# Performance work log

Hardware: AMD Instinct MI355X
Metric: run time of the kernel (lower is better)

The kernel has to match this reference:

```python
import jax, jax.numpy as jnp
import numpy as np

N_NODES = 100000
N_EDGES = 1200000
D_FEAT = 64
THETA = (1.0, -0.8, 0.4, -0.1)  # polynomial coefficients, k = len(THETA)


def setup_inputs() -> dict:
    key = jax.random.key(0)
    k1, k2, k3 = jax.random.split(key, 3)
    feat = jax.random.normal(k1, (N_NODES, D_FEAT), dtype=jnp.float32)
    src = jax.random.randint(k2, (N_EDGES,), 0, N_NODES, dtype=jnp.int32)
    dst = jax.random.randint(k3, (N_EDGES,), 0, N_NODES, dtype=jnp.int32)
    return {"feat": feat, "src": src, "dst": dst}


def reference(feat, src, dst):
    # in-degrees: number of incoming edges per node (clamped to >= 1)
    deg = jax.ops.segment_sum(jnp.ones((N_EDGES,), feat.dtype), dst, num_segments=N_NODES)
    d_invsqrt = jnp.clip(deg, 1.0, None) ** -0.5  # [N]
    d = d_invsqrt[:, None]  # [N, 1]

    h = THETA[0] * feat
    for k in range(1, len(THETA)):
        # unnLaplacian: feat - D^{-1/2} A^T (D^{-1/2} feat)  (copy_u / sum over edges)
        msg = (feat * d)[src]                                   # [E, F] gather
        agg = jax.ops.segment_sum(msg, dst, num_segments=N_NODES)  # [N, F] scatter-add
        feat = feat - agg * d
        h = h + THETA[k] * feat
    return h
```

## Files before the change

### kernel.cpp

```cpp
#include <hip/hip_runtime.h>

#define D_FEAT 64
#define BSHIFT 8
#define BNODES 256
#define CAP 3520
#define MAXB 512
#define CHUNK 4096

typedef float nfloat4 __attribute__((ext_vector_type(4)));

__device__ inline unsigned short f2bf(float f) {
    unsigned u = __float_as_uint(f);
    unsigned r = u + 0x7fffu + ((u >> 16) & 1u);
    return (unsigned short)(r >> 16);
}
__device__ inline float bflo(unsigned w) { return __uint_as_float(w << 16); }
__device__ inline float bfhi(unsigned w) { return __uint_as_float(w & 0xffff0000u); }

__device__ inline void unpack8(uint4 u, float* v) {
    v[0] = bflo(u.x); v[1] = bfhi(u.x);
    v[2] = bflo(u.y); v[3] = bfhi(u.y);
    v[4] = bflo(u.z); v[5] = bfhi(u.z);
    v[6] = bflo(u.w); v[7] = bfhi(u.w);
}
__device__ inline uint4 pack8(const float* v) {
    uint4 u;
    u.x = (unsigned)f2bf(v[0]) | ((unsigned)f2bf(v[1]) << 16);
    u.y = (unsigned)f2bf(v[2]) | ((unsigned)f2bf(v[3]) << 16);
    u.z = (unsigned)f2bf(v[4]) | ((unsigned)f2bf(v[5]) << 16);
    u.w = (unsigned)f2bf(v[6]) | ((unsigned)f2bf(v[7]) << 16);
    return u;
}

__global__ void initcur_kernel(int* __restrict__ cursor, int P) {
    int i = blockIdx.x * 256 + threadIdx.x;
    if (i < P) cursor[i] = i * CAP;
}

__global__ void scatter_kernel(const int* __restrict__ src, const int* __restrict__ dst,
                               int* __restrict__ cursor, unsigned* __restrict__ part,
                               int nE, int P) {
    __shared__ int lh[MAXB];
    __shared__ int lcur[MAXB];
    int tid = threadIdx.x;
    for (int i = tid; i < P; i += 256) lh[i] = 0;
    __syncthreads();
    int s = blockIdx.x * CHUNK;
    int e1 = s + CHUNK; if (e1 > nE) e1 = nE;
    for (int e = s + tid; e < e1; e += 256)
        atomicAdd(&lh[dst[e] >> BSHIFT], 1);
    __syncthreads();
    for (int i = tid; i < P; i += 256) {
        int c = lh[i];
        lcur[i] = c ? atomicAdd(&cursor[i], c) : 0;
    }
    __syncthreads();
    for (int e = s + tid; e < e1; e += 256) {
        int t = dst[e];
        int pos = atomicAdd(&lcur[t >> BSHIFT], 1);
        part[pos] = ((unsigned)src[e] << BSHIFT) | (unsigned)(t & (BNODES - 1));
    }
}

__global__ void bucket_csr_kernel(const unsigned* __restrict__ part,
                                  const int* __restrict__ cursor,
                                  int* __restrict__ row_ptr, int* __restrict__ row_end,
                                  float* __restrict__ dv, int* __restrict__ esrc,
                                  const float4* __restrict__ f,
                                  uint4* __restrict__ g0, uint4* __restrict__ g1,
                                  uint4* __restrict__ g2, int nN) {
    __shared__ int hist[BNODES];
    __shared__ int cur[BNODES];
    __shared__ int scanT[BNODES];
    __shared__ float sdv[BNODES];
    int b = blockIdx.x;
    int tid = threadIdx.x;
    int bp0 = b * CAP, bp1 = cursor[b];
    hist[tid] = 0;
    __syncthreads();
    for (int e = bp0 + tid; e < bp1; e += 256)
        atomicAdd(&hist[part[e] & (BNODES - 1)], 1);
    __syncthreads();
    int v = hist[tid];
    scanT[tid] = v;
    __syncthreads();
    for (int off = 1; off < 256; off <<= 1) {
        int t2 = 0;
        if (tid >= off) t2 = scanT[tid - off];
        __syncthreads();
        scanT[tid] += t2;
        __syncthreads();
    }
    int startv = scanT[tid] - v;
    cur[tid] = bp0 + startv;
    int node = (b << BSHIFT) + tid;
    float dt = 1.0f;
    if (node < nN) {
        float fc = (float)(v < 1 ? 1 : v);
        dt = rsqrtf(fc);
        dv[node] = dt;
        row_ptr[node] = bp0 + startv;
        row_end[node] = bp0 + startv + v;
    }
    sdv[tid] = dt;
    __syncthreads();
    for (int e = bp0 + tid; e < bp1; e += 256) {
        unsigned p = part[e];
        int rank = atomicAdd(&cur[p & (BNODES - 1)], 1);
        esrc[rank] = (int)(p >> BSHIFT);
    }
#pragma unroll
    for (int it = 0; it < 8; ++it) {
        int task = it * 256 + tid;
        int ln = task >> 3, q = task & 7;
        int nd = (b << BSHIFT) + ln;
        if (nd < nN) {
            float dl = sdv[ln];
            float4 a = f[(size_t)nd * 16 + q * 2];
            float4 c = f[(size_t)nd * 16 + q * 2 + 1];
            float vv[8] = {a.x * dl, a.y * dl, a.z * dl, a.w * dl,
                           c.x * dl, c.y * dl, c.z * dl, c.w * dl};
            g0[(size_t)nd * 8 + q] = pack8(vv);
        }
    }
    if (b == 0 && tid < 8) {
        uint4 z; z.x = z.y = z.z = z.w = 0u;
        g0[(size_t)nN * 8 + tid] = z;
        g1[(size_t)nN * 8 + tid] = z;
        g2[(size_t)nN * 8 + tid] = z;
    }
}

__global__ void poly_kernel(const uint4* __restrict__ g_in, uint4* __restrict__ g_out,
                            const int* __restrict__ row_ptr, const int* __restrict__ row_end,
                            const int* __restrict__ esrc, const float* __restrict__ dv,
                            const uint4* __restrict__ g0a, const uint4* __restrict__ g1a,
                            float* __restrict__ h, int final_step, int nN) {
    int wave = (blockIdx.x * blockDim.x + threadIdx.x) >> 6;
    int lane = threadIdx.x & 63;
    int sub  = lane >> 3;
    int q    = lane & 7;
    int t    = wave * 8 + sub;
    bool valid = (t < nN);
    if (!valid) t = nN - 1;

    int r0 = row_ptr[t], r1 = row_end[t];
    if (!valid) r1 = r0;

    float acc[8];
#pragma unroll
    for (int c = 0; c < 8; ++c) acc[c] = 0.0f;

    int sq = nN;
    { int jc = r0 + q; if (jc < r1) sq = esrc[jc]; }
    int j0 = r0;
    while (j0 < r1) {
        int jn = j0 + 8;
        int sq_n = nN;
        { int jc = jn + q; if (jc < r1) sq_n = esrc[jc]; }
        int m = r1 - j0;
#pragma unroll
        for (int u = 0; u < 4; ++u) {
            int sb = __shfl(sq, (sub << 3) + u, 64);
            uint4 fv = g_in[(size_t)sb * 8 + q];
            float v[8];
            unpack8(fv, v);
#pragma unroll
            for (int c = 0; c < 8; ++c) acc[c] += v[c];
        }
        if (m > 4) {
#pragma unroll
            for (int u = 4; u < 8; ++u) {
                int sb = __shfl(sq, (sub << 3) + u, 64);
                uint4 fv = g_in[(size_t)sb * 8 + q];
                float v[8];
                unpack8(fv, v);
#pragma unroll
                for (int c = 0; c < 8; ++c) acc[c] += v[c];
            }
        }
        sq = sq_n; j0 = jn;
    }

    if (!valid) return;
    size_t idx = (size_t)t * 8 + q;
    float dt = dv[t];
    float d2 = dt * dt;
    float go[8];
    unpack8(g_in[idx], go);
    float gn[8];
#pragma unroll
    for (int c = 0; c < 8; ++c) gn[c] = go[c] - acc[c] * d2;

    if (!final_step) {
        g_out[idx] = pack8(gn);
    } else {
        float g1v[8];
        unpack8(g1a[idx], g1v);
        float g0v[8];
        unpack8(g0a[idx], g0v);
        float di = 1.0f / dt;
        float hv[8];
#pragma unroll
        for (int c = 0; c < 8; ++c)
            hv[c] = (g0v[c] - 0.8f * g1v[c] + 0.4f * go[c] - 0.1f * gn[c]) * di;
        nfloat4 h0 = {hv[0], hv[1], hv[2], hv[3]};
        nfloat4 h1 = {hv[4], hv[5], hv[6], hv[7]};
        nfloat4* hp = (nfloat4*)(h + (size_t)t * 64 + q * 8);
        __builtin_nontemporal_store(h0, hp);
        __builtin_nontemporal_store(h1, hp + 1);
    }
}

extern "C" void kernel_launch(void* const* d_in, const int* in_sizes, int n_in,
                              void* d_out, int out_size, void* d_ws, size_t ws_size,
                              hipStream_t stream) {
    const float* feat = (const float*)d_in[0];
    const int*   src  = (const int*)d_in[1];
    const int*   dst  = (const int*)d_in[2];
    float*       h    = (float*)d_out;

    const int nN = in_sizes[0] / D_FEAT;
    const int nE = in_sizes[1];

    const int P    = (nN + BNODES - 1) >> BSHIFT;
    const int nblk = (nE + CHUNK - 1) / CHUNK;

    auto align = [](size_t x) { return (x + 255) & ~(size_t)255; };
    char* ws = (char*)d_ws;
    size_t off = 0;
    int*      cursor  = (int*)(ws + off);      off += align((size_t)P * 4);
    float*    dv      = (float*)(ws + off);    off += align((size_t)nN * 4);
    int*      row_ptr = (int*)(ws + off);      off += align((size_t)nN * 4);
    int*      row_end = (int*)(ws + off);      off += align((size_t)nN * 4);
    unsigned* part    = (unsigned*)(ws + off); off += align((size_t)P * CAP * 4);
    int*      esrc    = (int*)(ws + off);      off += align((size_t)P * CAP * 4);
    size_t fbBytes = (size_t)(nN + 1) * D_FEAT * 2;
    uint4*    fb0     = (uint4*)(ws + off);    off += align(fbBytes);
    uint4*    fb1     = (uint4*)(ws + off);    off += align(fbBytes);
    uint4*    fb2;
    if (ws_size >= off + fbBytes) {
        fb2 = (uint4*)(ws + off);
    } else {
        fb2 = (uint4*)d_in[0];
    }

    const int icb = (P + 255) / 256;
    initcur_kernel<<<icb, 256, 0, stream>>>(cursor, P);
    scatter_kernel<<<nblk, 256, 0, stream>>>(src, dst, cursor, part, nE, P);
    bucket_csr_kernel<<<P, 256, 0, stream>>>(part, cursor, row_ptr, row_end,
                                             dv, esrc, (const float4*)feat,
                                             fb0, fb1, fb2, nN);

    long long waves = ((long long)nN + 7) / 8;
    int polyBlocks = (int)((waves * 64 + 255) / 256);
    poly_kernel<<<polyBlocks, 256, 0, stream>>>(fb0, fb1, row_ptr, row_end, esrc, dv,
                                                nullptr, nullptr, nullptr, 0, nN);
    poly_kernel<<<polyBlocks, 256, 0, stream>>>(fb1, fb2, row_ptr, row_end, esrc, dv,
                                                nullptr, nullptr, nullptr, 0, nN);
    poly_kernel<<<polyBlocks, 256, 0, stream>>>(fb2, nullptr, row_ptr, row_end, esrc, dv,
                                                fb0, fb1, h, 1, nN);
}
```

Baseline: 192.2 us.

## Split bf16 feature buffers into two 32-column halves processed in separate passes

Lays each bf16 feature buffer out as two planes of 32 features per node and runs the three propagation steps once per half. Each gathered row segment becomes 64 bytes instead of 128, so the working set of one pass is halved and fits better in L2/MALL during the random gathers. Each wave now handles 16 nodes with 4 lanes each, and the loop consumes 4 edges per iteration. The cost is reading the CSR indices twice and launching six poly kernels instead of three.

```diff
diff --git a/kernel.cpp b/kernel.cpp
--- a/kernel.cpp
+++ b/kernel.cpp
@@ -73,6 +73,7 @@
     __shared__ int cur[BNODES];
     __shared__ int scanT[BNODES];
     __shared__ float sdv[BNODES];
+    size_t PS = (size_t)(nN + 1) * 4;
     int b = blockIdx.x;
     int tid = threadIdx.x;
     int bp0 = b * CAP, bp1 = cursor[b];
@@ -120,14 +121,13 @@
             float4 c = f[(size_t)nd * 16 + q * 2 + 1];
             float vv[8] = {a.x * dl, a.y * dl, a.z * dl, a.w * dl,
                            c.x * dl, c.y * dl, c.z * dl, c.w * dl};
-            g0[(size_t)nd * 8 + q] = pack8(vv);
+            g0[(size_t)(q >> 2) * PS + (size_t)nd * 4 + (q & 3)] = pack8(vv);
         }
     }
     if (b == 0 && tid < 8) {
         uint4 z; z.x = z.y = z.z = z.w = 0u;
-        g0[(size_t)nN * 8 + tid] = z;
-        g1[(size_t)nN * 8 + tid] = z;
-        g2[(size_t)nN * 8 + tid] = z;
+        size_t zi = (size_t)(tid >> 2) * PS + (size_t)nN * 4 + (tid & 3);
+        g0[zi] = z; g1[zi] = z; g2[zi] = z;
     }
 }
 
@@ -135,12 +135,12 @@
                             const int* __restrict__ row_ptr, const int* __restrict__ row_end,
                             const int* __restrict__ esrc, const float* __restrict__ dv,
                             const uint4* __restrict__ g0a, const uint4* __restrict__ g1a,
-                            float* __restrict__ h, int final_step, int nN) {
+                            float* __restrict__ h, int final_step, int hoff, int nN) {
     int wave = (blockIdx.x * blockDim.x + threadIdx.x) >> 6;
     int lane = threadIdx.x & 63;
-    int sub  = lane >> 3;
-    int q    = lane & 7;
-    int t    = wave * 8 + sub;
+    int sub  = lane >> 2;
+    int q    = lane & 3;
+    int t    = wave * 16 + sub;
     bool valid = (t < nN);
     if (!valid) t = nN - 1;
 
@@ -155,35 +155,23 @@
     { int jc = r0 + q; if (jc < r1) sq = esrc[jc]; }
     int j0 = r0;
     while (j0 < r1) {
-        int jn = j0 + 8;
+        int jn = j0 + 4;
         int sq_n = nN;
         { int jc = jn + q; if (jc < r1) sq_n = esrc[jc]; }
-        int m = r1 - j0;
 #pragma unroll
         for (int u = 0; u < 4; ++u) {
-            int sb = __shfl(sq, (sub << 3) + u, 64);
-            uint4 fv = g_in[(size_t)sb * 8 + q];
+            int sb = __shfl(sq, (sub << 2) + u, 64);
+            uint4 fv = g_in[(size_t)sb * 4 + q];
             float v[8];
             unpack8(fv, v);
 #pragma unroll
             for (int c = 0; c < 8; ++c) acc[c] += v[c];
         }
-        if (m > 4) {
-#pragma unroll
-            for (int u = 4; u < 8; ++u) {
-                int sb = __shfl(sq, (sub << 3) + u, 64);
-                uint4 fv = g_in[(size_t)sb * 8 + q];
-                float v[8];
-                unpack8(fv, v);
-#pragma unroll
-                for (int c = 0; c < 8; ++c) acc[c] += v[c];
-            }
-        }
         sq = sq_n; j0 = jn;
     }
 
     if (!valid) return;
-    size_t idx = (size_t)t * 8 + q;
+    size_t idx = (size_t)t * 4 + q;
     float dt = dv[t];
     float d2 = dt * dt;
     float go[8];
@@ -206,7 +194,7 @@
             hv[c] = (g0v[c] - 0.8f * g1v[c] + 0.4f * go[c] - 0.1f * gn[c]) * di;
         nfloat4 h0 = {hv[0], hv[1], hv[2], hv[3]};
         nfloat4 h1 = {hv[4], hv[5], hv[6], hv[7]};
-        nfloat4* hp = (nfloat4*)(h + (size_t)t * 64 + q * 8);
+        nfloat4* hp = (nfloat4*)(h + (size_t)t * 64 + hoff + q * 8);
         __builtin_nontemporal_store(h0, hp);
         __builtin_nontemporal_store(h1, hp + 1);
     }
@@ -252,12 +240,18 @@
                                              dv, esrc, (const float4*)feat,
                                              fb0, fb1, fb2, nN);
 
-    long long waves = ((long long)nN + 7) / 8;
+    long long waves = ((long long)nN + 15) / 16;
     int polyBlocks = (int)((waves * 64 + 255) / 256);
-    poly_kernel<<<polyBlocks, 256, 0, stream>>>(fb0, fb1, row_ptr, row_end, esrc, dv,
-                                                nullptr, nullptr, nullptr, 0, nN);
-    poly_kernel<<<polyBlocks, 256, 0, stream>>>(fb1, fb2, row_ptr, row_end, esrc, dv,
-                                                nullptr, nullptr, nullptr, 0, nN);
-    poly_kernel<<<polyBlocks, 256, 0, stream>>>(fb2, nullptr, row_ptr, row_end, esrc, dv,
-                                                fb0, fb1, h, 1, nN);
-}
+    size_t PS = (size_t)(nN + 1) * 4;
+    for (int p = 0; p < 2; ++p) {
+        const uint4* f0p = fb0 + (size_t)p * PS;
+        uint4*       f1p = fb1 + (size_t)p * PS;
+        uint4*       f2p = fb2 + (size_t)p * PS;
+        poly_kernel<<<polyBlocks, 256, 0, stream>>>(f0p, f1p, row_ptr, row_end, esrc, dv,
+                                                    nullptr, nullptr, nullptr, 0, 0, nN);
+        poly_kernel<<<polyBlocks, 256, 0, stream>>>(f1p, f2p, row_ptr, row_end, esrc, dv,
+                                                    nullptr, nullptr, nullptr, 0, 0, nN);
+        poly_kernel<<<polyBlocks, 256, 0, stream>>>(f2p, nullptr, row_ptr, row_end, esrc, dv,
+                                                    f0p, f1p, h, 1, p * 32, nN);
+    }
+}
```

Result: slower. 223.9 us (+16.5%).

## Gather FP8 feature copies in later polynomial steps with 16 nodes per wave

Applied to the files above, without the earlier changes.

Each propagation step now also writes an FP8 (e4m3) copy of the new features alongside the bf16 copy. The second and third steps gather neighbour rows from the FP8 copy, 64 bytes per row instead of 128, and use a new layout of 4 lanes per node, 16 nodes per wave. This roughly halves the random-gather traffic in those steps. The cost is an extra FP8 write per step and much coarser precision in the aggregated values, which may break accuracy tolerances.

```diff
diff --git a/kernel.cpp b/kernel.cpp
--- a/kernel.cpp
+++ b/kernel.cpp
@@ -32,6 +32,15 @@
     return u;
 }
 
+__device__ inline uint2 packf8(const float* v) {
+    int w0 = __builtin_amdgcn_cvt_pk_fp8_f32(v[0], v[1], 0, false);
+    w0 = __builtin_amdgcn_cvt_pk_fp8_f32(v[2], v[3], w0, true);
+    int w1 = __builtin_amdgcn_cvt_pk_fp8_f32(v[4], v[5], 0, false);
+    w1 = __builtin_amdgcn_cvt_pk_fp8_f32(v[6], v[7], w1, true);
+    uint2 r; r.x = (unsigned)w0; r.y = (unsigned)w1;
+    return r;
+}
+
 __global__ void initcur_kernel(int* __restrict__ cursor, int P) {
     int i = blockIdx.x * 256 + threadIdx.x;
     if (i < P) cursor[i] = i * CAP;
@@ -68,7 +77,9 @@
                                   float* __restrict__ dv, int* __restrict__ esrc,
                                   const float4* __restrict__ f,
                                   uint4* __restrict__ g0, uint4* __restrict__ g1,
-                                  uint4* __restrict__ g2, int nN) {
+                                  uint4* __restrict__ g2,
+                                  uint4* __restrict__ g1f8, uint4* __restrict__ g2f8,
+                                  int nN) {
     __shared__ int hist[BNODES];
     __shared__ int cur[BNODES];
     __shared__ int scanT[BNODES];
@@ -128,14 +139,18 @@
         g0[(size_t)nN * 8 + tid] = z;
         g1[(size_t)nN * 8 + tid] = z;
         g2[(size_t)nN * 8 + tid] = z;
-    }
-}
-
-__global__ void poly_kernel(const uint4* __restrict__ g_in, uint4* __restrict__ g_out,
-                            const int* __restrict__ row_ptr, const int* __restrict__ row_end,
-                            const int* __restrict__ esrc, const float* __restrict__ dv,
-                            const uint4* __restrict__ g0a, const uint4* __restrict__ g1a,
-                            float* __restrict__ h, int final_step, int nN) {
+        if (tid < 4) {
+            g1f8[(size_t)nN * 4 + tid] = z;
+            g2f8[(size_t)nN * 4 + tid] = z;
+        }
+    }
+}
+
+__global__ void poly_bf_kernel(const uint4* __restrict__ g_in, uint4* __restrict__ g_out,
+                               uint2* __restrict__ f8out,
+                               const int* __restrict__ row_ptr, const int* __restrict__ row_end,
+                               const int* __restrict__ esrc, const float* __restrict__ dv,
+                               int nN) {
     int wave = (blockIdx.x * blockDim.x + threadIdx.x) >> 6;
     int lane = threadIdx.x & 63;
     int sub  = lane >> 3;
@@ -191,24 +206,102 @@
     float gn[8];
 #pragma unroll
     for (int c = 0; c < 8; ++c) gn[c] = go[c] - acc[c] * d2;
+    g_out[idx] = pack8(gn);
+    f8out[idx] = packf8(gn);
+}
+
+__global__ void poly_f8_kernel(const uint4* __restrict__ f8in,
+                               const uint4* __restrict__ gbf_in,
+                               uint4* __restrict__ gbf_out, uint4* __restrict__ f8out,
+                               const int* __restrict__ row_ptr, const int* __restrict__ row_end,
+                               const int* __restrict__ esrc, const float* __restrict__ dv,
+                               const uint4* __restrict__ g0a, const uint4* __restrict__ g1a,
+                               float* __restrict__ h, int final_step, int nN) {
+    int wave = (blockIdx.x * blockDim.x + threadIdx.x) >> 6;
+    int lane = threadIdx.x & 63;
+    int sub  = lane >> 2;
+    int qq   = lane & 3;
+    int t    = wave * 16 + sub;
+    bool valid = (t < nN);
+    if (!valid) t = nN - 1;
+
+    int r0 = row_ptr[t], r1 = row_end[t];
+    if (!valid) r1 = r0;
+
+    float acc[16];
+#pragma unroll
+    for (int c = 0; c < 16; ++c) acc[c] = 0.0f;
+
+    int sqA = nN, sqB = nN;
+    { int jc = r0 + qq;     if (jc < r1) sqA = esrc[jc]; }
+    { int jc = r0 + 4 + qq; if (jc < r1) sqB = esrc[jc]; }
+    int j0 = r0;
+    while (j0 < r1) {
+        int jn = j0 + 8;
+        int sqA_n = nN, sqB_n = nN;
+        { int jc = jn + qq;     if (jc < r1) sqA_n = esrc[jc]; }
+        { int jc = jn + 4 + qq; if (jc < r1) sqB_n = esrc[jc]; }
+#pragma unroll
+        for (int u = 0; u < 8; ++u) {
+            int sv = (u < 4) ? sqA : sqB;
+            int sb = __shfl(sv, (sub << 2) + (u & 3), 64);
+            uint4 fv = f8in[(size_t)sb * 4 + qq];
+            acc[0]  += __builtin_amdgcn_cvt_f32_fp8((int)fv.x, 0);
+            acc[1]  += __builtin_amdgcn_cvt_f32_fp8((int)fv.x, 1);
+            acc[2]  += __builtin_amdgcn_cvt_f32_fp8((int)fv.x, 2);
+            acc[3]  += __builtin_amdgcn_cvt_f32_fp8((int)fv.x, 3);
+            acc[4]  += __builtin_amdgcn_cvt_f32_fp8((int)fv.y, 0);
+            acc[5]  += __builtin_amdgcn_cvt_f32_fp8((int)fv.y, 1);
+            acc[6]  += __builtin_amdgcn_cvt_f32_fp8((int)fv.y, 2);
+            acc[7]  += __builtin_amdgcn_cvt_f32_fp8((int)fv.y, 3);
+            acc[8]  += __builtin_amdgcn_cvt_f32_fp8((int)fv.z, 0);
+            acc[9]  += __builtin_amdgcn_cvt_f32_fp8((int)fv.z, 1);
+            acc[10] += __builtin_amdgcn_cvt_f32_fp8((int)fv.z, 2);
+            acc[11] += __builtin_amdgcn_cvt_f32_fp8((int)fv.z, 3);
+            acc[12] += __builtin_amdgcn_cvt_f32_fp8((int)fv.w, 0);
+            acc[13] += __builtin_amdgcn_cvt_f32_fp8((int)fv.w, 1);
+            acc[14] += __builtin_amdgcn_cvt_f32_fp8((int)fv.w, 2);
+            acc[15] += __builtin_amdgcn_cvt_f32_fp8((int)fv.w, 3);
+        }
+        sqA = sqA_n; sqB = sqB_n; j0 = jn;
+    }
+
+    if (!valid) return;
+    size_t idx8 = (size_t)t * 8 + qq * 2;
+    float dt = dv[t];
+    float d2 = dt * dt;
+    float go[16];
+    unpack8(gbf_in[idx8], go);
+    unpack8(gbf_in[idx8 + 1], go + 8);
+    float gn[16];
+#pragma unroll
+    for (int c = 0; c < 16; ++c) gn[c] = go[c] - acc[c] * d2;
 
     if (!final_step) {
-        g_out[idx] = pack8(gn);
+        gbf_out[idx8]     = pack8(gn);
+        gbf_out[idx8 + 1] = pack8(gn + 8);
+        uint2 lo = packf8(gn);
+        uint2 hi = packf8(gn + 8);
+        uint4 pw; pw.x = lo.x; pw.y = lo.y; pw.z = hi.x; pw.w = hi.y;
+        f8out[(size_t)t * 4 + qq] = pw;
     } else {
-        float g1v[8];
-        unpack8(g1a[idx], g1v);
-        float g0v[8];
-        unpack8(g0a[idx], g0v);
+        float g1v[16];
+        unpack8(g1a[idx8], g1v);
+        unpack8(g1a[idx8 + 1], g1v + 8);
+        float g0v[16];
+        unpack8(g0a[idx8], g0v);
+        unpack8(g0a[idx8 + 1], g0v + 8);
         float di = 1.0f / dt;
-        float hv[8];
-#pragma unroll
-        for (int c = 0; c < 8; ++c)
+        float hv[16];
+#pragma unroll
+        for (int c = 0; c < 16; ++c)
             hv[c] = (g0v[c] - 0.8f * g1v[c] + 0.4f * go[c] - 0.1f * gn[c]) * di;
-        nfloat4 h0 = {hv[0], hv[1], hv[2], hv[3]};
-        nfloat4 h1 = {hv[4], hv[5], hv[6], hv[7]};
-        nfloat4* hp = (nfloat4*)(h + (size_t)t * 64 + q * 8);
-        __builtin_nontemporal_store(h0, hp);
-        __builtin_nontemporal_store(h1, hp + 1);
+        nfloat4* hp = (nfloat4*)(h + (size_t)t * 64 + qq * 16);
+#pragma unroll
+        for (int w = 0; w < 4; ++w) {
+            nfloat4 hw = {hv[w * 4], hv[w * 4 + 1], hv[w * 4 + 2], hv[w * 4 + 3]};
+            __builtin_nontemporal_store(hw, hp + w);
+        }
     }
 }
 
@@ -235,6 +328,9 @@
     int*      row_end = (int*)(ws + off);      off += align((size_t)nN * 4);
     unsigned* part    = (unsigned*)(ws + off); off += align((size_t)P * CAP * 4);
     int*      esrc    = (int*)(ws + off);      off += align((size_t)P * CAP * 4);
+    size_t f8Bytes = (size_t)(nN + 1) * D_FEAT;
+    uint4*    g1f8    = (uint4*)(ws + off);    off += align(f8Bytes);
+    uint4*    g2f8    = (uint4*)(ws + off);    off += align(f8Bytes);
     size_t fbBytes = (size_t)(nN + 1) * D_FEAT * 2;
     uint4*    fb0     = (uint4*)(ws + off);    off += align(fbBytes);
     uint4*    fb1     = (uint4*)(ws + off);    off += align(fbBytes);
@@ -250,14 +346,19 @@
     scatter_kernel<<<nblk, 256, 0, stream>>>(src, dst, cursor, part, nE, P);
     bucket_csr_kernel<<<P, 256, 0, stream>>>(part, cursor, row_ptr, row_end,
                                              dv, esrc, (const float4*)feat,
-                                             fb0, fb1, fb2, nN);
-
-    long long waves = ((long long)nN + 7) / 8;
-    int polyBlocks = (int)((waves * 64 + 255) / 256);
-    poly_kernel<<<polyBlocks, 256, 0, stream>>>(fb0, fb1, row_ptr, row_end, esrc, dv,
-                                                nullptr, nullptr, nullptr, 0, nN);
-    poly_kernel<<<polyBlocks, 256, 0, stream>>>(fb1, fb2, row_ptr, row_end, esrc, dv,
-                                                nullptr, nullptr, nullptr, 0, nN);
-    poly_kernel<<<polyBlocks, 256, 0, stream>>>(fb2, nullptr, row_ptr, row_end, esrc, dv,
-                                                fb0, fb1, h, 1, nN);
-}
+                                             fb0, fb1, fb2, g1f8, g2f8, nN);
+
+    long long waves8 = ((long long)nN + 7) / 8;
+    int blocks8 = (int)((waves8 * 64 + 255) / 256);
+    poly_bf_kernel<<<blocks8, 256, 0, stream>>>(fb0, fb1, (uint2*)g1f8,
+                                                row_ptr, row_end, esrc, dv, nN);
+
+    long long waves16 = ((long long)nN + 15) / 16;
+    int blocks16 = (int)((waves16 * 64 + 255) / 256);
+    poly_f8_kernel<<<blocks16, 256, 0, stream>>>(g1f8, fb1, fb2, g2f8,
+                                                 row_ptr, row_end, esrc, dv,
+                                                 nullptr, nullptr, nullptr, 0, nN);
+    poly_f8_kernel<<<blocks16, 256, 0, stream>>>(g2f8, fb2, nullptr, nullptr,
+                                                 row_ptr, row_end, esrc, dv,
+                                                 fb0, fb1, h, 1, nN);
+}
```

After: 280.8 us. +46.1%, slower.
